# Optimization experiments

Hardware: AMD Instinct MI355X
Metric: run time of the kernel (lower is better)

## Reference

```python
import jax, jax.numpy as jnp
import numpy as np

FEAT_STRIDE = 16
ANCHOR_SCALES = (8.0, 16.0, 32.0)
ANCHOR_RATIOS = (0.5, 1.0, 2.0)
PRE_NMS_TOPN = 12000
POST_NMS_TOPN = 2000
NMS_THRESH = 0.7
MIN_SIZE = 16.0


def _mkanchors(ws, hs, cx, cy):
    return np.stack([cx - 0.5 * (ws - 1), cy - 0.5 * (hs - 1),
                     cx + 0.5 * (ws - 1), cy + 0.5 * (hs - 1)], axis=1)


def generate_anchors(base_size=16, ratios=ANCHOR_RATIOS, scales=ANCHOR_SCALES):
    ratios = np.asarray(ratios, np.float32)
    scales = np.asarray(scales, np.float32)
    w = h = float(base_size)
    cx = cy = 0.5 * (base_size - 1)
    size = w * h
    ws = np.round(np.sqrt(size / ratios))
    hs = np.round(ws * ratios)
    ratio_anchors = _mkanchors(ws, hs, cx, cy)
    out = []
    for a in ratio_anchors:
        aw = a[2] - a[0] + 1.0
        ah = a[3] - a[1] + 1.0
        acx = a[0] + 0.5 * (aw - 1)
        acy = a[1] + 0.5 * (ah - 1)
        out.append(_mkanchors(aw * scales, ah * scales, acx, acy))
    return np.concatenate(out, axis=0).astype(np.float32)  # (A, 4)


ANCHORS = generate_anchors(FEAT_STRIDE)
NUM_ANCHORS = ANCHORS.shape[0]  # 9


def _proposal_forward(scores, bbox_deltas, im_info):
    A = NUM_ANCHORS
    fg = scores[:, A:, :, :]                       # (1, A, H, W) foreground scores
    H, W = fg.shape[-2], fg.shape[-1]
    im_h, im_w, im_scale = im_info[0, 0], im_info[0, 1], im_info[0, 2]

    # anchor grid
    sx = jnp.arange(W, dtype=jnp.float32) * FEAT_STRIDE
    sy = jnp.arange(H, dtype=jnp.float32) * FEAT_STRIDE
    gy, gx = jnp.meshgrid(sy, sx, indexing='ij')
    shifts = jnp.stack([gx.ravel(), gy.ravel(), gx.ravel(), gy.ravel()], axis=1)  # (K,4)
    anchors = jnp.asarray(ANCHORS)[None, :, :] + shifts[:, None, :]
    anchors = anchors.reshape(-1, 4)               # (K*A, 4)

    deltas = jnp.transpose(bbox_deltas, (0, 2, 3, 1)).reshape(-1, 4)
    sc = jnp.transpose(fg, (0, 2, 3, 1)).reshape(-1)

    # bbox_transform_inv
    aw = anchors[:, 2] - anchors[:, 0] + 1.0
    ah = anchors[:, 3] - anchors[:, 1] + 1.0
    acx = anchors[:, 0] + 0.5 * aw
    acy = anchors[:, 1] + 0.5 * ah
    pcx = deltas[:, 0] * aw + acx
    pcy = deltas[:, 1] * ah + acy
    pw = jnp.exp(deltas[:, 2]) * aw
    ph = jnp.exp(deltas[:, 3]) * ah
    x1 = pcx - 0.5 * pw
    y1 = pcy - 0.5 * ph
    x2 = pcx + 0.5 * pw
    y2 = pcy + 0.5 * ph

    # clip_boxes (scale slot in the clip call is 1.0 in the original)
    x1 = jnp.clip(x1, 0.0, im_w - 1.0)
    x2 = jnp.clip(x2, 0.0, im_w - 1.0)
    y1 = jnp.clip(y1, 0.0, im_h - 1.0)
    y2 = jnp.clip(y2, 0.0, im_h - 1.0)
    props = jnp.stack([x1, y1, x2, y2], axis=1)

    # _filter_boxes: mask instead of gather (jit-safe fixed shapes)
    ms = MIN_SIZE * im_scale
    valid = ((x2 - x1 + 1.0) >= ms) & ((y2 - y1 + 1.0) >= ms)
    sc_m = jnp.where(valid, sc, -jnp.inf)

    # descending sort + pre-NMS top-k in one shot
    top_sc, order = jax.lax.top_k(sc_m, PRE_NMS_TOPN)
    p = props[order]                               # (preN, 4) sorted by score desc
    vk = valid[order]

    pn = jax.lax.stop_gradient(p)
    areas = (pn[:, 2] - pn[:, 0] + 1.0) * (pn[:, 3] - pn[:, 1] + 1.0)
    xx1 = jnp.maximum(pn[:, 0][:, None], pn[:, 0][None, :])
    yy1 = jnp.maximum(pn[:, 1][:, None], pn[:, 1][None, :])
    xx2 = jnp.minimum(pn[:, 2][:, None], pn[:, 2][None, :])
    yy2 = jnp.minimum(pn[:, 3][:, None], pn[:, 3][None, :])
    inter = jnp.maximum(xx2 - xx1 + 1.0, 0.0) * jnp.maximum(yy2 - yy1 + 1.0, 0.0)
    iou = inter / (areas[:, None] + areas[None, :] - inter)
    sup_mat = iou > NMS_THRESH                     # (preN, preN) bool

    idx = jnp.arange(PRE_NMS_TOPN, dtype=jnp.int32)

    def body(keep, xs):
        sup_row, i = xs
        keep = jnp.where(keep[i], keep & ~(sup_row & (idx > i)), keep)
        return keep, None

    keep, _ = jax.lax.scan(body, vk, (sup_mat, idx))

    # keep[:post_nms_topN] with fixed shapes: rank kept boxes, scatter into slots
    rank = jnp.cumsum(keep.astype(jnp.int32)) - 1
    slot_src = jnp.where(keep & (rank < POST_NMS_TOPN), rank, POST_NMS_TOPN)
    slots = jnp.full((POST_NMS_TOPN,), PRE_NMS_TOPN, jnp.int32).at[slot_src].set(idx, mode='drop')

    p_pad = jnp.concatenate([p, jnp.zeros((1, 4), p.dtype)], axis=0)
    s_pad = jnp.concatenate([top_sc, jnp.zeros((1,), top_sc.dtype)], axis=0)
    boxes = p_pad[slots]
    out_sc = s_pad[slots][:, None]
    rois = jnp.concatenate([jnp.zeros((POST_NMS_TOPN, 1), boxes.dtype), boxes], axis=1)
    return rois, out_sc


def setup_inputs() -> dict:
    key = jax.random.key(0)
    k1, k2 = jax.random.split(key)
    H = W = 512
    scores = jax.random.normal(k1, (1, 2 * NUM_ANCHORS, H, W), jnp.float32)
    bbox_deltas = jax.random.normal(k2, (1, 4 * NUM_ANCHORS, H, W), jnp.float32) * 0.2
    im_info = jnp.array([[float(H * FEAT_STRIDE), float(W * FEAT_STRIDE), 1.0]], jnp.float32)
    return {"scores": scores, "bbox_deltas": bbox_deltas, "im_info": im_info}


def reference(scores, bbox_deltas, im_info):
    return _proposal_forward(scores, bbox_deltas, im_info)
```

## Files before the change

### kernel.cpp

```cpp
#include <hip/hip_runtime.h>
#include <hip/hip_bf16.h>
#include <stdint.h>

#pragma clang fp contract(off)

#define FH 512
#define FW 512
#define NA 9
#define HW (FH*FW)
#define TOTAL (HW*NA)
#define PRE_NMS 12000
#define POST_NMS 2000
#define NMS_WORDS 188
#define MT 12032
#define CAND_MAX 16384
#define NMS_TH 0.7f
#define MIN_SIZE_C 16.0f

__constant__ float ANCH[NA][4] = {
  {-84.f,-40.f,99.f,55.f},
  {-176.f,-88.f,191.f,103.f},
  {-360.f,-184.f,375.f,199.f},
  {-56.f,-56.f,71.f,71.f},
  {-120.f,-120.f,135.f,135.f},
  {-248.f,-248.f,263.f,263.f},
  {-36.f,-80.f,51.f,95.f},
  {-80.f,-168.f,95.f,183.f},
  {-168.f,-344.f,183.f,359.f}
};

__device__ __forceinline__ void decode_box(int a, int h, int w,
    const float* __restrict__ deltas, float im_h, float im_w,
    float& x1, float& y1, float& x2, float& y2) {
  float sx = (float)(w * 16);
  float sy = (float)(h * 16);
  float ax1 = ANCH[a][0] + sx;
  float ay1 = ANCH[a][1] + sy;
  float ax2 = ANCH[a][2] + sx;
  float ay2 = ANCH[a][3] + sy;
  float aw = ax2 - ax1 + 1.0f;
  float ah = ay2 - ay1 + 1.0f;
  float acx = ax1 + 0.5f * aw;
  float acy = ay1 + 0.5f * ah;
  int base = h * FW + w;
  float d0 = deltas[(4*a+0)*HW + base];
  float d1 = deltas[(4*a+1)*HW + base];
  float d2 = deltas[(4*a+2)*HW + base];
  float d3 = deltas[(4*a+3)*HW + base];
  float pcx = d0 * aw + acx;
  float pcy = d1 * ah + acy;
  float pw = expf(d2) * aw;
  float ph = expf(d3) * ah;
  x1 = pcx - 0.5f * pw;
  y1 = pcy - 0.5f * ph;
  x2 = pcx + 0.5f * pw;
  y2 = pcy + 0.5f * ph;
  x1 = fminf(fmaxf(x1, 0.0f), im_w - 1.0f);
  x2 = fminf(fmaxf(x2, 0.0f), im_w - 1.0f);
  y1 = fminf(fmaxf(y1, 0.0f), im_h - 1.0f);
  y2 = fminf(fmaxf(y2, 0.0f), im_h - 1.0f);
}

__global__ void k_keys(const float* __restrict__ scores, const float* __restrict__ deltas,
                       const float* __restrict__ im_info, unsigned* __restrict__ keys,
                       unsigned* __restrict__ hist8) {
  __shared__ unsigned lh[256];
  int t = threadIdx.x;
  lh[t] = 0;
  __syncthreads();
  int base = blockIdx.x * blockDim.x + t;
  float im_h = im_info[0], im_w = im_info[1];
  float ms = MIN_SIZE_C * im_info[2];
  int h = base / FW, w = base % FW;
  for (int a = 0; a < NA; a++) {
    float x1, y1, x2, y2;
    decode_box(a, h, w, deltas, im_h, im_w, x1, y1, x2, y2);
    bool valid = ((x2 - x1 + 1.0f) >= ms) && ((y2 - y1 + 1.0f) >= ms);
    float sc = scores[(NA + a)*HW + base];
    float v = valid ? sc : -INFINITY;
    unsigned u = __float_as_uint(v);
    unsigned mono = (u & 0x80000000u) ? ~u : (u | 0x80000000u);
    keys[base*NA + a] = mono;
    atomicAdd(&lh[mono >> 24], 1u);
  }
  __syncthreads();
  atomicAdd(&hist8[t], lh[t]);
}

__global__ void __launch_bounds__(256) k_refine15(const unsigned* __restrict__ keys,
    const unsigned* __restrict__ hist8, unsigned* __restrict__ hist15) {
  __shared__ unsigned ssum[256];
  __shared__ unsigned sB8;
  int t = threadIdx.x;
  unsigned hv = hist8[t];
  ssum[t] = hv;
  __syncthreads();
  for (int off = 1; off < 256; off <<= 1) {
    unsigned v = ssum[t];
    unsigned add = (t + off < 256) ? ssum[t + off] : 0u;
    __syncthreads();
    ssum[t] = v + add;
    __syncthreads();
  }
  unsigned above = ssum[t] - hv;
  if (above < PRE_NMS && above + hv >= PRE_NMS) sB8 = (unsigned)t;
  __syncthreads();
  unsigned B8 = sB8;
  int stride = gridDim.x * blockDim.x;
  for (int i = blockIdx.x * blockDim.x + t; i < TOTAL; i += stride) {
    unsigned k = keys[i];
    if ((k >> 24) == B8) atomicAdd(&hist15[(k >> 9) & 0x7FFFu], 1u);
  }
}

__global__ void __launch_bounds__(256) k_compact(const unsigned* __restrict__ keys,
    const unsigned* __restrict__ hist8, const unsigned* __restrict__ hist15,
    unsigned* __restrict__ cnt, unsigned long long* __restrict__ cand) {
  __shared__ unsigned ssum[256];
  __shared__ unsigned sB8, sT2, sB15;
  int t = threadIdx.x;
  unsigned hv = hist8[t];
  ssum[t] = hv;
  __syncthreads();
  for (int off = 1; off < 256; off <<= 1) {
    unsigned v = ssum[t];
    unsigned add = (t + off < 256) ? ssum[t + off] : 0u;
    __syncthreads();
    ssum[t] = v + add;
    __syncthreads();
  }
  unsigned above = ssum[t] - hv;
  if (above < PRE_NMS && above + hv >= PRE_NMS) { sB8 = (unsigned)t; sT2 = PRE_NMS - above; }
  __syncthreads();
  unsigned B8 = sB8, T2 = sT2;
  unsigned loc = 0;
  for (int i = 0; i < 128; i++) loc += hist15[t*128 + i];
  __syncthreads();
  ssum[t] = loc;
  __syncthreads();
  for (int off = 1; off < 256; off <<= 1) {
    unsigned v = ssum[t];
    unsigned add = (t + off < 256) ? ssum[t + off] : 0u;
    __syncthreads();
    ssum[t] = v + add;
    __syncthreads();
  }
  unsigned above15 = ssum[t] - loc;
  unsigned acc = above15;
  for (int i = 127; i >= 0; i--) {
    unsigned cb = hist15[t*128 + i];
    acc += cb;
    if (acc >= T2 && acc - cb < T2) sB15 = (unsigned)(t*128 + i);
  }
  __syncthreads();
  unsigned K = (B8 << 24) | (sB15 << 9);
  int stride = gridDim.x * blockDim.x;
  for (int i = blockIdx.x * blockDim.x + t; i < TOTAL; i += stride) {
    unsigned k = keys[i];
    if (k >= K) {
      unsigned pos = atomicAdd(cnt, 1u);
      if (pos < CAND_MAX)
        cand[pos] = ((unsigned long long)k << 32) | (unsigned)(~(unsigned)i);
    }
  }
}

__global__ void __launch_bounds__(256) k_rank(const unsigned* __restrict__ pcnt,
    const unsigned long long* __restrict__ cand,
    const float* __restrict__ deltas, const float* __restrict__ im_info,
    float4* __restrict__ boxes, float* __restrict__ scoresArr,
    unsigned long long* __restrict__ remvInit) {
  __shared__ unsigned long long tile[2048];
  unsigned cnt = *pcnt;
  if (cnt > CAND_MAX) cnt = CAND_MAX;
  int i = blockIdx.x * 256 + threadIdx.x;
  unsigned long long mine = (i < (int)cnt) ? cand[i] : 0ULL;
  int rank = 0;
  for (unsigned t0 = 0; t0 < cnt; t0 += 2048) {
    unsigned n = min(2048u, cnt - t0);
    __syncthreads();
    for (unsigned j = threadIdx.x; j < n; j += 256) tile[j] = cand[t0 + j];
    __syncthreads();
    if (i < (int)cnt) {
      unsigned j = 0;
      #pragma unroll 8
      for (; j < n; j++) rank += (tile[j] > mine) ? 1 : 0;
    }
  }
  if (i < (int)cnt && rank < PRE_NMS) {
    unsigned mono = (unsigned)(mine >> 32);
    unsigned idx = ~(unsigned)(mine & 0xFFFFFFFFull);
    unsigned u = (mono & 0x80000000u) ? (mono ^ 0x80000000u) : ~mono;
    float sc = __uint_as_float(u);
    int a = idx % NA;
    int base = idx / NA;
    int h = base / FW, w = base % FW;
    float x1, y1, x2, y2;
    decode_box(a, h, w, deltas, im_info[0], im_info[1], x1, y1, x2, y2);
    boxes[rank] = make_float4(x1, y1, x2, y2);
    scoresArr[rank] = sc;
    if (!(sc > -INFINITY)) atomicOr(&remvInit[rank >> 6], 1ULL << (rank & 63));
  }
}

__global__ void k_mask(const float4* __restrict__ boxes, unsigned long long* __restrict__ maskT) {
  int bi = blockIdx.y, bj = blockIdx.x;
  if (bj < bi) return;
  __shared__ float4 jb[64];
  int t = threadIdx.x;
  int jg = bj * 64 + t;
  jb[t] = (jg < PRE_NMS) ? boxes[jg] : make_float4(0.f, 0.f, -1.f, -1.f);
  __syncthreads();
  int i = bi * 64 + t;
  if (i >= PRE_NMS) return;
  float4 b = boxes[i];
  float area_i = (b.z - b.x + 1.0f) * (b.w - b.y + 1.0f);
  unsigned long long bits = 0;
  for (int jj = 0; jj < 64; jj++) {
    float4 o = jb[jj];
    float xx1 = fmaxf(b.x, o.x);
    float yy1 = fmaxf(b.y, o.y);
    float xx2 = fminf(b.z, o.z);
    float yy2 = fminf(b.w, o.w);
    float iw = fmaxf(xx2 - xx1 + 1.0f, 0.0f);
    float ih = fmaxf(yy2 - yy1 + 1.0f, 0.0f);
    float inter = iw * ih;
    float area_o = (o.z - o.x + 1.0f) * (o.w - o.y + 1.0f);
    float iou = inter / (area_i + area_o - inter);
    if (iou > NMS_TH) bits |= (1ULL << jj);
  }
  maskT[(size_t)bj * MT + i] = bits;
}

__global__ void __launch_bounds__(64) k_nms(const unsigned long long* __restrict__ maskT,
    const unsigned long long* __restrict__ remvInit,
    const float4* __restrict__ boxes, const float* __restrict__ scoresArr,
    float* __restrict__ out) {
  int lane = threadIdx.x;
  __shared__ unsigned klist[POST_NMS];
  __shared__ unsigned long long gbuf[32 * 128];
  int kept_cnt = 0;
  bool done = false;
  unsigned long long W = remvInit[0];
  unsigned long long diagc = maskT[lane];
  unsigned long long nwc   = maskT[(size_t)MT + lane];
  for (int c = 0; c < NMS_WORDS; c++) {
    bool more = (c + 1 < NMS_WORDS);
    int kc = kept_cnt;
    int nIss = more ? ((kc + 63) >> 6) : 0;
    for (int ii = 0; ii < nIss; ii++) {
      int q = ii * 64 + lane;
      if (q < kc) {
        unsigned j = klist[q];
        const void* g = (const void*)(maskT + (size_t)(c + 1) * MT + (j & ~1u));
        void* l = (void*)((char*)gbuf + ii * 1024);
        __builtin_amdgcn_global_load_lds(
            (const __attribute__((address_space(1))) unsigned*)g,
            (__attribute__((address_space(3))) unsigned*)l, 16, 0, 0);
      }
    }
    unsigned long long diagN = 0, nwN = 0;
    if (more) {
      diagN = maskT[(size_t)(c + 1) * MT + (c + 1) * 64 + lane];
      if (c + 2 < NMS_WORDS) nwN = maskT[(size_t)(c + 2) * MT + (c + 1) * 64 + lane];
    }
    int gi0 = c * 64;
    int jmax = PRE_NMS - gi0; if (jmax > 64) jmax = 64;
    unsigned long long avail = ~W;
    if (jmax < 64) avail &= ((1ULL << jmax) - 1ULL);
    unsigned long long keptmask = 0;
    while (avail) {
      int j = __ffsll((long long)avail) - 1;
      keptmask |= (1ULL << j);
      if (lane == 0) klist[kept_cnt] = (unsigned)(gi0 + j);
      kept_cnt++;
      if (kept_cnt >= POST_NMS) { done = true; break; }
      unsigned long long supp = __shfl(diagc, j);
      avail &= ~supp;
      avail &= ~((2ULL << j) - 1ULL);
    }
    if (done || !more) break;
    unsigned long long x = ((keptmask >> lane) & 1ULL) ? nwc : 0ULL;
    asm volatile("s_waitcnt vmcnt(0)" ::: "memory");
    for (int ii = 0; ii < nIss; ii++) {
      int q = ii * 64 + lane;
      if (q < kc) {
        unsigned j = klist[q];
        x |= gbuf[ii * 128 + lane * 2 + (j & 1u)];
      }
    }
    for (int off = 32; off; off >>= 1) x |= __shfl_xor(x, off);
    W = x | remvInit[c + 1];
    __syncthreads();
    diagc = diagN; nwc = nwN;
  }
  __syncthreads();
  for (int s = lane; s < POST_NMS; s += 64) {
    float x1 = 0.f, y1 = 0.f, x2 = 0.f, y2 = 0.f, sc = 0.f;
    if (s < kept_cnt) {
      unsigned r = klist[s];
      float4 b = boxes[r];
      x1 = b.x; y1 = b.y; x2 = b.z; y2 = b.w;
      sc = scoresArr[r];
    }
    out[s*5 + 0] = 0.f;
    out[s*5 + 1] = x1;
    out[s*5 + 2] = y1;
    out[s*5 + 3] = x2;
    out[s*5 + 4] = y2;
    out[POST_NMS*5 + s] = sc;
  }
}

extern "C" void kernel_launch(void* const* d_in, const int* in_sizes, int n_in,
                              void* d_out, int out_size, void* d_ws, size_t ws_size,
                              hipStream_t stream) {
  const float* scores  = (const float*)d_in[0];
  const float* deltas  = (const float*)d_in[1];
  const float* im_info = (const float*)d_in[2];
  float* out = (float*)d_out;
  char* ws = (char*)d_ws;

  unsigned* keys             = (unsigned*)(ws + 0);
  unsigned* hist8            = (unsigned*)(ws + 9437184);
  unsigned* hist15           = (unsigned*)(ws + 9438208);
  unsigned* scal             = (unsigned*)(ws + 9569280);
  unsigned long long* remvI  = (unsigned long long*)(ws + 9569536);
  unsigned long long* cand   = (unsigned long long*)(ws + 9571072);
  float4* boxes              = (float4*)(ws + 9702144);
  float* scoresArr           = (float*)(ws + 9894144);
  unsigned long long* maskT  = (unsigned long long*)(ws + 9942144);

  hipMemsetAsync(ws + 9437184, 0, 133888, stream);

  k_keys<<<HW/256, 256, 0, stream>>>(scores, deltas, im_info, keys, hist8);
  k_refine15<<<256, 256, 0, stream>>>(keys, hist8, hist15);
  k_compact<<<256, 256, 0, stream>>>(keys, hist8, hist15, &scal[4], cand);
  k_rank<<<CAND_MAX/256, 256, 0, stream>>>(&scal[4], cand, deltas, im_info,
                                           boxes, scoresArr, remvI);
  dim3 mg(NMS_WORDS, NMS_WORDS);
  k_mask<<<mg, 64, 0, stream>>>(boxes, maskT);
  k_nms<<<1, 64, 0, stream>>>(maskT, remvI, boxes, scoresArr, out);
}
```

Baseline: 907.2 us.

## Rework keys layout, rank split, row-major NMS mask and multi-wave NMS pipeline

Measured after the change: 853.2 us. -6.0%, faster.

```diff
diff --git a/kernel.cpp b/kernel.cpp
--- a/kernel.cpp
+++ b/kernel.cpp
@@ -3,6 +3,8 @@
 #include <stdint.h>
 
 #pragma clang fp contract(off)
+
+typedef unsigned long long u64;
 
 #define FH 512
 #define FW 512
@@ -12,7 +14,7 @@
 #define PRE_NMS 12000
 #define POST_NMS 2000
 #define NMS_WORDS 188
-#define MT 12032
+#define MROW 192
 #define CAND_MAX 16384
 #define NMS_TH 0.7f
 #define MIN_SIZE_C 16.0f
@@ -61,6 +63,12 @@
   y2 = fminf(fmaxf(y2, 0.0f), im_h - 1.0f);
 }
 
+__device__ __forceinline__ u64 rl64(u64 v, int l) {
+  unsigned lo = (unsigned)__builtin_amdgcn_readlane((int)(unsigned)(v & 0xFFFFFFFFull), l);
+  unsigned hi = (unsigned)__builtin_amdgcn_readlane((int)(unsigned)(v >> 32), l);
+  return ((u64)hi << 32) | lo;
+}
+
 __global__ void k_keys(const float* __restrict__ scores, const float* __restrict__ deltas,
                        const float* __restrict__ im_info, unsigned* __restrict__ keys,
                        unsigned* __restrict__ hist8) {
@@ -71,7 +79,7 @@
   int base = blockIdx.x * blockDim.x + t;
   float im_h = im_info[0], im_w = im_info[1];
   float ms = MIN_SIZE_C * im_info[2];
-  int h = base / FW, w = base % FW;
+  int h = base >> 9, w = base & 511;
   for (int a = 0; a < NA; a++) {
     float x1, y1, x2, y2;
     decode_box(a, h, w, deltas, im_h, im_w, x1, y1, x2, y2);
@@ -80,7 +88,7 @@
     float v = valid ? sc : -INFINITY;
     unsigned u = __float_as_uint(v);
     unsigned mono = (u & 0x80000000u) ? ~u : (u | 0x80000000u);
-    keys[base*NA + a] = mono;
+    keys[a*HW + base] = mono;
     atomicAdd(&lh[mono >> 24], 1u);
   }
   __syncthreads();
@@ -115,7 +123,7 @@
 
 __global__ void __launch_bounds__(256) k_compact(const unsigned* __restrict__ keys,
     const unsigned* __restrict__ hist8, const unsigned* __restrict__ hist15,
-    unsigned* __restrict__ cnt, unsigned long long* __restrict__ cand) {
+    unsigned* __restrict__ cnt, u64* __restrict__ cand) {
   __shared__ unsigned ssum[256];
   __shared__ unsigned sB8, sT2, sB15;
   int t = threadIdx.x;
@@ -159,145 +167,185 @@
     unsigned k = keys[i];
     if (k >= K) {
       unsigned pos = atomicAdd(cnt, 1u);
-      if (pos < CAND_MAX)
-        cand[pos] = ((unsigned long long)k << 32) | (unsigned)(~(unsigned)i);
-    }
-  }
-}
-
-__global__ void __launch_bounds__(256) k_rank(const unsigned* __restrict__ pcnt,
-    const unsigned long long* __restrict__ cand,
+      if (pos < CAND_MAX) {
+        unsigned a = ((unsigned)i) >> 18;
+        unsigned base2 = ((unsigned)i) & 262143u;
+        unsigned oi = base2 * 9u + a;
+        cand[pos] = ((u64)k << 32) | (unsigned)(~oi);
+      }
+    }
+  }
+}
+
+__global__ void __launch_bounds__(1024) k_rankdec(const unsigned* __restrict__ pcnt,
+    const u64* __restrict__ cand,
     const float* __restrict__ deltas, const float* __restrict__ im_info,
     float4* __restrict__ boxes, float* __restrict__ scoresArr,
-    unsigned long long* __restrict__ remvInit) {
-  __shared__ unsigned long long tile[2048];
+    u64* __restrict__ remvI) {
+  __shared__ u64 tile[2048];
+  __shared__ unsigned part[256][4];
   unsigned cnt = *pcnt;
   if (cnt > CAND_MAX) cnt = CAND_MAX;
-  int i = blockIdx.x * 256 + threadIdx.x;
-  unsigned long long mine = (i < (int)cnt) ? cand[i] : 0ULL;
-  int rank = 0;
+  int t = threadIdx.x;
+  int iq = t & 255, qw = t >> 8;
+  int i = blockIdx.x * 256 + iq;
+  u64 mine = (i < (int)cnt) ? cand[i] : ~0ULL;
+  unsigned pr = 0;
   for (unsigned t0 = 0; t0 < cnt; t0 += 2048) {
     unsigned n = min(2048u, cnt - t0);
     __syncthreads();
-    for (unsigned j = threadIdx.x; j < n; j += 256) tile[j] = cand[t0 + j];
+    for (unsigned j = t; j < n; j += 1024) tile[j] = cand[t0 + j];
     __syncthreads();
     if (i < (int)cnt) {
-      unsigned j = 0;
-      #pragma unroll 8
-      for (; j < n; j++) rank += (tile[j] > mine) ? 1 : 0;
-    }
-  }
-  if (i < (int)cnt && rank < PRE_NMS) {
-    unsigned mono = (unsigned)(mine >> 32);
-    unsigned idx = ~(unsigned)(mine & 0xFFFFFFFFull);
-    unsigned u = (mono & 0x80000000u) ? (mono ^ 0x80000000u) : ~mono;
-    float sc = __uint_as_float(u);
-    int a = idx % NA;
-    int base = idx / NA;
-    int h = base / FW, w = base % FW;
-    float x1, y1, x2, y2;
-    decode_box(a, h, w, deltas, im_info[0], im_info[1], x1, y1, x2, y2);
-    boxes[rank] = make_float4(x1, y1, x2, y2);
-    scoresArr[rank] = sc;
-    if (!(sc > -INFINITY)) atomicOr(&remvInit[rank >> 6], 1ULL << (rank & 63));
-  }
-}
-
-__global__ void k_mask(const float4* __restrict__ boxes, unsigned long long* __restrict__ maskT) {
-  int bi = blockIdx.y, bj = blockIdx.x;
-  if (bj < bi) return;
-  __shared__ float4 jb[64];
-  int t = threadIdx.x;
-  int jg = bj * 64 + t;
-  jb[t] = (jg < PRE_NMS) ? boxes[jg] : make_float4(0.f, 0.f, -1.f, -1.f);
-  __syncthreads();
-  int i = bi * 64 + t;
-  if (i >= PRE_NMS) return;
+      unsigned j0 = qw * 512;
+      unsigned j1 = min(j0 + 512, n);
+      for (unsigned j = j0; j < j1; j++) pr += (tile[j] > mine) ? 1u : 0u;
+    }
+  }
+  part[iq][qw] = pr;
+  __syncthreads();
+  if (t < 256 && (blockIdx.x * 256 + t) < (int)cnt) {
+    unsigned rank = part[t][0] + part[t][1] + part[t][2] + part[t][3];
+    if (rank < PRE_NMS) {
+      u64 m = cand[blockIdx.x * 256 + t];
+      unsigned mono = (unsigned)(m >> 32);
+      unsigned idx = ~(unsigned)(m & 0xFFFFFFFFull);
+      unsigned u = (mono & 0x80000000u) ? (mono ^ 0x80000000u) : ~mono;
+      float sc = __uint_as_float(u);
+      int a = idx % NA;
+      int base = idx / NA;
+      int h = base / FW, w = base % FW;
+      float x1, y1, x2, y2;
+      decode_box(a, h, w, deltas, im_info[0], im_info[1], x1, y1, x2, y2);
+      boxes[rank] = make_float4(x1, y1, x2, y2);
+      scoresArr[rank] = sc;
+      if (sc > -INFINITY)
+        atomicAnd(&remvI[rank >> 6], ~(1ULL << (rank & 63)));
+    }
+  }
+}
+
+__global__ void __launch_bounds__(256) k_mask(const float4* __restrict__ boxes,
+                                              u64* __restrict__ mask) {
+  int wg = blockIdx.x;
+  int bg = blockIdx.y;
+  if (wg * 8 + 7 < bg * 4) return;
+  __shared__ float4 jb[512];
+  int t = threadIdx.x;
+  for (int q = t; q < 512; q += 256) {
+    int jg = wg * 512 + q;
+    jb[q] = (jg < PRE_NMS) ? boxes[jg] : make_float4(0.f, 0.f, -1.f, -1.f);
+  }
+  __syncthreads();
+  int i = bg * 256 + t;
+  if (i >= PRE_NMS || wg * 8 + 7 < (i >> 6)) return;
   float4 b = boxes[i];
   float area_i = (b.z - b.x + 1.0f) * (b.w - b.y + 1.0f);
-  unsigned long long bits = 0;
-  for (int jj = 0; jj < 64; jj++) {
-    float4 o = jb[jj];
-    float xx1 = fmaxf(b.x, o.x);
-    float yy1 = fmaxf(b.y, o.y);
-    float xx2 = fminf(b.z, o.z);
-    float yy2 = fminf(b.w, o.w);
-    float iw = fmaxf(xx2 - xx1 + 1.0f, 0.0f);
-    float ih = fmaxf(yy2 - yy1 + 1.0f, 0.0f);
-    float inter = iw * ih;
-    float area_o = (o.z - o.x + 1.0f) * (o.w - o.y + 1.0f);
-    float iou = inter / (area_i + area_o - inter);
-    if (iou > NMS_TH) bits |= (1ULL << jj);
-  }
-  maskT[(size_t)bj * MT + i] = bits;
-}
-
-__global__ void __launch_bounds__(64) k_nms(const unsigned long long* __restrict__ maskT,
-    const unsigned long long* __restrict__ remvInit,
+  u64 bits[8];
+  #pragma unroll
+  for (int k = 0; k < 8; k++) {
+    u64 bb = 0;
+    for (int jj = 0; jj < 64; jj++) {
+      float4 o = jb[k * 64 + jj];
+      float xx1 = fmaxf(b.x, o.x);
+      float yy1 = fmaxf(b.y, o.y);
+      float xx2 = fminf(b.z, o.z);
+      float yy2 = fminf(b.w, o.w);
+      float iw = fmaxf(xx2 - xx1 + 1.0f, 0.0f);
+      float ih = fmaxf(yy2 - yy1 + 1.0f, 0.0f);
+      float inter = iw * ih;
+      float area_o = (o.z - o.x + 1.0f) * (o.w - o.y + 1.0f);
+      float iou = inter / (area_i + area_o - inter);
+      if (iou > NMS_TH) bb |= (1ULL << jj);
+    }
+    bits[k] = bb;
+  }
+  size_t rb = (size_t)i * MROW + wg * 8;
+  #pragma unroll
+  for (int k = 0; k < 8; k++) mask[rb + k] = bits[k];
+}
+
+__global__ void __launch_bounds__(512) k_nms(const u64* __restrict__ mask,
+    const u64* __restrict__ remvI,
     const float4* __restrict__ boxes, const float* __restrict__ scoresArr,
     float* __restrict__ out) {
-  int lane = threadIdx.x;
+  __shared__ unsigned R32[384];
   __shared__ unsigned klist[POST_NMS];
-  __shared__ unsigned long long gbuf[32 * 128];
-  int kept_cnt = 0;
-  bool done = false;
-  unsigned long long W = remvInit[0];
-  unsigned long long diagc = maskT[lane];
-  unsigned long long nwc   = maskT[(size_t)MT + lane];
+  __shared__ int sPub[2][2];
+  __shared__ int sDone, sKept;
+  int t = threadIdx.x;
+  int lane = t & 63, wv = t >> 6;
+  for (int w = t; w < 384; w += 512) R32[w] = ((const unsigned*)remvI)[w];
+  if (t == 0) { sDone = 0; sPub[0][0] = sPub[0][1] = sPub[1][0] = sPub[1][1] = 0; }
+  __syncthreads();
+  u64 diag0 = 0, nw10 = 0, diag1 = 0, nw11 = 0, A = 0;
+  int kept = 0;
+  if (wv == 0) {
+    diag0 = mask[(size_t)lane * MROW + 0];
+    nw10  = mask[(size_t)lane * MROW + 1];
+    diag1 = mask[(size_t)(64 + lane) * MROW + 1];
+    nw11  = mask[(size_t)(64 + lane) * MROW + 2];
+  }
   for (int c = 0; c < NMS_WORDS; c++) {
-    bool more = (c + 1 < NMS_WORDS);
-    int kc = kept_cnt;
-    int nIss = more ? ((kc + 63) >> 6) : 0;
-    for (int ii = 0; ii < nIss; ii++) {
-      int q = ii * 64 + lane;
-      if (q < kc) {
-        unsigned j = klist[q];
-        const void* g = (const void*)(maskT + (size_t)(c + 1) * MT + (j & ~1u));
-        void* l = (void*)((char*)gbuf + ii * 1024);
-        __builtin_amdgcn_global_load_lds(
-            (const __attribute__((address_space(1))) unsigned*)g,
-            (__attribute__((address_space(3))) unsigned*)l, 16, 0, 0);
-      }
-    }
-    unsigned long long diagN = 0, nwN = 0;
-    if (more) {
-      diagN = maskT[(size_t)(c + 1) * MT + (c + 1) * 64 + lane];
-      if (c + 2 < NMS_WORDS) nwN = maskT[(size_t)(c + 2) * MT + (c + 1) * 64 + lane];
-    }
-    int gi0 = c * 64;
-    int jmax = PRE_NMS - gi0; if (jmax > 64) jmax = 64;
-    unsigned long long avail = ~W;
-    if (jmax < 64) avail &= ((1ULL << jmax) - 1ULL);
-    unsigned long long keptmask = 0;
-    while (avail) {
-      int j = __ffsll((long long)avail) - 1;
-      keptmask |= (1ULL << j);
-      if (lane == 0) klist[kept_cnt] = (unsigned)(gi0 + j);
-      kept_cnt++;
-      if (kept_cnt >= POST_NMS) { done = true; break; }
-      unsigned long long supp = __shfl(diagc, j);
-      avail &= ~supp;
-      avail &= ~((2ULL << j) - 1ULL);
-    }
-    if (done || !more) break;
-    unsigned long long x = ((keptmask >> lane) & 1ULL) ? nwc : 0ULL;
-    asm volatile("s_waitcnt vmcnt(0)" ::: "memory");
-    for (int ii = 0; ii < nIss; ii++) {
-      int q = ii * 64 + lane;
-      if (q < kc) {
-        unsigned j = klist[q];
-        x |= gbuf[ii * 128 + lane * 2 + (j & 1u)];
-      }
-    }
-    for (int off = 32; off; off >>= 1) x |= __shfl_xor(x, off);
-    W = x | remvInit[c + 1];
-    __syncthreads();
-    diagc = diagN; nwc = nwN;
-  }
-  __syncthreads();
-  for (int s = lane; s < POST_NMS; s += 64) {
+    if (wv == 0) {
+      int gi0 = c * 64;
+      int jmax = PRE_NMS - gi0; if (jmax > 64) jmax = 64;
+      u64 Rc = ((u64)R32[2*c + 1] << 32) | R32[2*c];
+      u64 avail = ~(Rc | A);
+      if (jmax < 64) avail &= ((1ULL << jmax) - 1ULL);
+      A = 0;
+      int st = kept;
+      bool done = false;
+      while (avail) {
+        int j = __ffsll((long long)avail) - 1;
+        if (lane == 0) klist[kept] = (unsigned)(gi0 + j);
+        kept++;
+        if (kept >= POST_NMS) { done = true; break; }
+        u64 supp = rl64(diag0, j);
+        A |= rl64(nw10, j);
+        avail &= ~supp;
+        avail &= ~((2ULL << j) - 1ULL);
+      }
+      if (lane == 0) {
+        sPub[c & 1][0] = st; sPub[c & 1][1] = kept;
+        if (done || c == NMS_WORDS - 1) sDone = 1;
+      }
+      u64 d2 = 0, n2 = 0;
+      if (c + 2 < NMS_WORDS) {
+        size_t rb = (size_t)((c + 2) * 64 + lane) * MROW;
+        d2 = mask[rb + (c + 2)];
+        if (c + 3 < NMS_WORDS) n2 = mask[rb + (c + 3)];
+      }
+      diag0 = diag1; nw10 = nw11; diag1 = d2; nw11 = n2;
+    } else if (c > 0) {
+      int s0 = sPub[(c - 1) & 1][0], s1 = sPub[(c - 1) & 1][1];
+      u64 o0 = 0, o1 = 0, o2 = 0;
+      bool any = false;
+      for (int q = s0 + (wv - 1); q < s1; q += 7) {
+        const u64* rp = mask + (size_t)klist[q] * MROW;
+        o0 |= rp[lane];
+        o1 |= rp[64 + lane];
+        o2 |= rp[128 + lane];
+        any = true;
+      }
+      if (any) {
+        atomicOr(&R32[2*lane],             (unsigned)o0);
+        atomicOr(&R32[2*lane + 1],         (unsigned)(o0 >> 32));
+        atomicOr(&R32[2*(64 + lane)],      (unsigned)o1);
+        atomicOr(&R32[2*(64 + lane) + 1],  (unsigned)(o1 >> 32));
+        atomicOr(&R32[2*(128 + lane)],     (unsigned)o2);
+        atomicOr(&R32[2*(128 + lane) + 1], (unsigned)(o2 >> 32));
+      }
+    }
+    __syncthreads();
+    if (sDone) break;
+  }
+  if (t == 0) sKept = kept;
+  __syncthreads();
+  int kc = sKept;
+  for (int s = t; s < POST_NMS; s += 512) {
     float x1 = 0.f, y1 = 0.f, x2 = 0.f, y2 = 0.f, sc = 0.f;
-    if (s < kept_cnt) {
+    if (s < kc) {
       unsigned r = klist[s];
       float4 b = boxes[r];
       x1 = b.x; y1 = b.y; x2 = b.z; y2 = b.w;
@@ -321,24 +369,25 @@
   float* out = (float*)d_out;
   char* ws = (char*)d_ws;
 
-  unsigned* keys             = (unsigned*)(ws + 0);
-  unsigned* hist8            = (unsigned*)(ws + 9437184);
-  unsigned* hist15           = (unsigned*)(ws + 9438208);
-  unsigned* scal             = (unsigned*)(ws + 9569280);
-  unsigned long long* remvI  = (unsigned long long*)(ws + 9569536);
-  unsigned long long* cand   = (unsigned long long*)(ws + 9571072);
-  float4* boxes              = (float4*)(ws + 9702144);
-  float* scoresArr           = (float*)(ws + 9894144);
-  unsigned long long* maskT  = (unsigned long long*)(ws + 9942144);
-
-  hipMemsetAsync(ws + 9437184, 0, 133888, stream);
+  unsigned* keys    = (unsigned*)(ws + 0);
+  unsigned* hist8   = (unsigned*)(ws + 9437184);
+  unsigned* hist15  = (unsigned*)(ws + 9438208);
+  unsigned* scal    = (unsigned*)(ws + 9569280);
+  u64* remvI        = (u64*)(ws + 9569536);
+  u64* cand         = (u64*)(ws + 9571072);
+  float4* boxes     = (float4*)(ws + 9767680);
+  float* scoresArr  = (float*)(ws + 9960192);
+  u64* mask         = (u64*)(ws + 10008576);
+
+  hipMemsetAsync(ws + 9437184, 0, 132352, stream);
+  hipMemsetAsync(ws + 9569536, 0xFF, 1536, stream);
 
   k_keys<<<HW/256, 256, 0, stream>>>(scores, deltas, im_info, keys, hist8);
-  k_refine15<<<256, 256, 0, stream>>>(keys, hist8, hist15);
-  k_compact<<<256, 256, 0, stream>>>(keys, hist8, hist15, &scal[4], cand);
-  k_rank<<<CAND_MAX/256, 256, 0, stream>>>(&scal[4], cand, deltas, im_info,
-                                           boxes, scoresArr, remvI);
-  dim3 mg(NMS_WORDS, NMS_WORDS);
-  k_mask<<<mg, 64, 0, stream>>>(boxes, maskT);
-  k_nms<<<1, 64, 0, stream>>>(maskT, remvI, boxes, scoresArr, out);
-}
+  k_refine15<<<512, 256, 0, stream>>>(keys, hist8, hist15);
+  k_compact<<<512, 256, 0, stream>>>(keys, hist8, hist15, &scal[4], cand);
+  k_rankdec<<<CAND_MAX/256, 1024, 0, stream>>>(&scal[4], cand, deltas, im_info,
+                                               boxes, scoresArr, remvI);
+  dim3 mg(24, 47);
+  k_mask<<<mg, 256, 0, stream>>>(boxes, mask);
+  k_nms<<<1, 512, 0, stream>>>(mask, remvI, boxes, scoresArr, out);
+}
```
